# Performance work log

Measured on AMD Instinct MI355X. Metric: run time of the kernel, lower is better.

The kernel has to match this reference:

```python
import jax, jax.numpy as jnp
import numpy as np

TAU = 0.5  # temperature
W_SCALE = 1.0 / np.sqrt(2048.0)  # keep logits in a sane range (like nn.Linear init)


def setup_inputs() -> dict:
    key = jax.random.key(0)
    k1, k2, k3 = jax.random.split(key, 3)
    B, I, O, N = 8192, 2048, 256, 64
    x = jax.random.normal(k1, (B, I), dtype=jnp.float32)
    W = jax.random.normal(k2, (O, N, I), dtype=jnp.float32) * W_SCALE
    b = jnp.zeros((O, N), dtype=jnp.float32)
    grid = jnp.linspace(-1.0, 1.0, N, dtype=jnp.float32)
    # pre-sampled standard Gumbel noise (reparameterized sampling, fixed for determinism)
    u = jax.random.uniform(k3, (B, O, N), dtype=jnp.float32, minval=1e-6, maxval=1.0 - 1e-6)
    gumbel_noise = -jnp.log(-jnp.log(u))
    return {"x": x, "W": W, "b": b, "grid": grid, "gumbel_noise": gumbel_noise}


def reference(x, W, b, grid, gumbel_noise):
    B = x.shape[0]
    O, N, _ = W.shape
    # per-output-feature linears fused into one GEMM; stack(dim=-1) order -> [B, N, O]
    factors = jnp.einsum('bi,oni->bno', x, W) + b.T  # [B, n_bins, out_features]
    # torch .view(B, out_features, n_bins) on the contiguous stacked tensor == reshape
    factors_logits = factors.reshape(B, O, N)
    # gumbel-softmax sampling (soft), then collapse bins onto the value grid
    y = jax.nn.softmax((factors_logits + gumbel_noise) / TAU, axis=-1)  # [B, O, N]
    encoded = jnp.einsum('bon,n->bo', y, grid)  # [B, out_features]
    return (encoded, factors_logits)
```

## Files before the change

kernel.cpp:

```cpp
#include <hip/hip_runtime.h>
#include <hip/hip_bf16.h>
#include <stdint.h>

typedef __bf16 bf16x8 __attribute__((ext_vector_type(8)));
typedef float f32x4 __attribute__((ext_vector_type(4)));
typedef unsigned short u16x8 __attribute__((ext_vector_type(8)));

#define B_ROWS 8192
#define K_DIM  2048
#define O_DIM  256
#define N_BINS 64
#define J_DIM  (O_DIM * N_BINS)
#define NT     (K_DIM / 64)

__device__ __forceinline__ unsigned short f2bf(float f) {
    union { float f; unsigned u; } v; v.f = f;
    unsigned r = (v.u + 0x7fffu + ((v.u >> 16) & 1u)) >> 16;
    return (unsigned short)r;
}

__global__ void cvt_x_kernel(const float* __restrict__ x, unsigned short* __restrict__ xb) {
    int i = (blockIdx.x * 256 + threadIdx.x) * 4;
    float4 v = *(const float4*)(x + i);
    ushort4 o;
    o.x = f2bf(v.x); o.y = f2bf(v.y); o.z = f2bf(v.z); o.w = f2bf(v.w);
    *(ushort4*)(xb + i) = o;
}

__global__ void cvt_w_kernel(const float* __restrict__ W, unsigned short* __restrict__ vb) {
    int bid = blockIdx.x;
    int p   = bid >> 1;
    int i0  = (bid & 1) * 1024 + threadIdx.x * 4;
    int src = (p & (O_DIM - 1)) * (N_BINS * K_DIM) + (p >> 8) * K_DIM + i0;
    float4 v = *(const float4*)(W + src);
    ushort4 o;
    o.x = f2bf(v.x); o.y = f2bf(v.y); o.z = f2bf(v.z); o.w = f2bf(v.w);
    *(ushort4*)(vb + (size_t)p * K_DIM + i0) = o;
}

__device__ __forceinline__ u16x8 pack8(float4 a, float4 b) {
    u16x8 r;
    r[0] = f2bf(a.x); r[1] = f2bf(a.y); r[2] = f2bf(a.z); r[3] = f2bf(a.w);
    r[4] = f2bf(b.x); r[5] = f2bf(b.y); r[6] = f2bf(b.z); r[7] = f2bf(b.w);
    return r;
}

#define GLDS(gsrc, ldst) \
    __builtin_amdgcn_global_load_lds((const __attribute__((address_space(1))) void*)(gsrc), \
                                     (__attribute__((address_space(3))) void*)(ldst), 16, 0, 0)
#define SBAR()   __builtin_amdgcn_s_barrier()
#define SCHED0() __builtin_amdgcn_sched_barrier(0)
#define WAIT_VM(N)   do { asm volatile("s_waitcnt vmcnt(" #N ")" ::: "memory"); } while (0)
#define WAIT_LGKM0() do { asm volatile("s_waitcnt lgkmcnt(0)" ::: "memory"); SCHED0(); } while (0)
#define MFMA(a, b, c) (c) = __builtin_amdgcn_mfma_f32_16x16x32_bf16((a), (b), (c), 0, 0, 0)

__global__ __launch_bounds__(512, 2) void gemm8_kernel(
    const unsigned short* __restrict__ xb,
    const unsigned short* __restrict__ vb,
    const float* __restrict__ bias,
    float* __restrict__ logits)
{
    __shared__ unsigned short As[2][2][256][32];
    __shared__ unsigned short Bs[2][2][256][32];

    const int tid  = threadIdx.x;
    const int lane = tid & 63;
    const int wv   = tid >> 6;
    const int wr   = wv >> 2;
    const int wc   = wv & 3;

    const int bid = blockIdx.x;
    const int swz  = (bid & 7) * 256 + (bid >> 3);
    const int bm   = (swz >> 8) * 4 + (swz & 3);
    const int bn   = (swz & 255) >> 2;
    const int row0 = bm * 256;
    const int col0 = bn * 256;

    const int oss = (tid * 16) ^ (tid & 32);
    const int sr  = oss >> 6;
    const int sc  = (oss >> 1) & 31;

    const unsigned short* gA = xb + (size_t)(row0 + sr) * K_DIM + sc;
    const unsigned short* gB = vb + (size_t)(col0 + sr) * K_DIM + sc;

    auto stageA = [&](int kt, int h, int b) {
        const unsigned short* g = gA + kt * 64 + h * 32;
        unsigned short* l = &As[b][h][0][0] + wv * 512;
        GLDS(g, l);
        GLDS(g + (size_t)128 * K_DIM, l + 4096);
    };
    auto stageB = [&](int kt, int h, int b) {
        const unsigned short* g = gB + kt * 64 + h * 32;
        unsigned short* l = &Bs[b][h][0][0] + wv * 512;
        GLDS(g, l);
        GLDS(g + (size_t)128 * K_DIM, l + 4096);
    };

    const int arb  = wr * 128 + (lane & 15);
    const int brb  = wc * 64 + (lane & 15);
    const int slot = ((lane >> 4) * 8) ^ ((lane & 8) << 1);

    f32x4 acc[8][4];
#pragma unroll
    for (int m = 0; m < 8; ++m)
#pragma unroll
        for (int n = 0; n < 4; ++n)
            acc[m][n] = (f32x4){0.f, 0.f, 0.f, 0.f};

    bf16x8 af[8], b0, b1;

    stageA(0, 0, 0); stageB(0, 0, 0); stageA(0, 1, 0); stageB(0, 1, 0);
    WAIT_VM(4); SCHED0(); SBAR(); SCHED0();

    for (int kt = 0; kt < NT - 1; ++kt) {
        const int cur = kt & 1, nxt = cur ^ 1;
#pragma unroll
        for (int m = 0; m < 8; ++m) af[m] = *(const bf16x8*)&As[cur][0][arb + m * 16][slot];
        b0 = *(const bf16x8*)&Bs[cur][0][brb][slot];
        b1 = *(const bf16x8*)&Bs[cur][0][brb + 16][slot];
        stageA(kt + 1, 0, nxt);
        SBAR(); WAIT_LGKM0();
        __builtin_amdgcn_s_setprio(1);
#pragma unroll
        for (int m = 0; m < 8; ++m) { MFMA(af[m], b0, acc[m][0]); MFMA(af[m], b1, acc[m][1]); }
        __builtin_amdgcn_s_setprio(0);
        SBAR();
        b0 = *(const bf16x8*)&Bs[cur][0][brb + 32][slot];
        b1 = *(const bf16x8*)&Bs[cur][0][brb + 48][slot];
        stageB(kt + 1, 0, nxt);
        WAIT_VM(4); SCHED0(); SBAR(); SCHED0();
        WAIT_LGKM0();
        __builtin_amdgcn_s_setprio(1);
#pragma unroll
        for (int m = 0; m < 8; ++m) { MFMA(af[m], b0, acc[m][2]); MFMA(af[m], b1, acc[m][3]); }
        __builtin_amdgcn_s_setprio(0);
        SBAR();
#pragma unroll
        for (int m = 0; m < 8; ++m) af[m] = *(const bf16x8*)&As[cur][1][arb + m * 16][slot];
        b0 = *(const bf16x8*)&Bs[cur][1][brb + 32][slot];
        b1 = *(const bf16x8*)&Bs[cur][1][brb + 48][slot];
        stageA(kt + 1, 1, nxt);
        SBAR(); WAIT_LGKM0();
        __builtin_amdgcn_s_setprio(1);
#pragma unroll
        for (int m = 0; m < 8; ++m) { MFMA(af[m], b0, acc[m][2]); MFMA(af[m], b1, acc[m][3]); }
        __builtin_amdgcn_s_setprio(0);
        SBAR();
        b0 = *(const bf16x8*)&Bs[cur][1][brb][slot];
        b1 = *(const bf16x8*)&Bs[cur][1][brb + 16][slot];
        stageB(kt + 1, 1, nxt);
        WAIT_VM(4); SCHED0(); SBAR(); SCHED0();
        WAIT_LGKM0();
        __builtin_amdgcn_s_setprio(1);
#pragma unroll
        for (int m = 0; m < 8; ++m) { MFMA(af[m], b0, acc[m][0]); MFMA(af[m], b1, acc[m][1]); }
        __builtin_amdgcn_s_setprio(0);
        SBAR();
    }

    {
        const int cur = (NT - 1) & 1;
#pragma unroll
        for (int m = 0; m < 8; ++m) af[m] = *(const bf16x8*)&As[cur][0][arb + m * 16][slot];
        b0 = *(const bf16x8*)&Bs[cur][0][brb][slot];
        b1 = *(const bf16x8*)&Bs[cur][0][brb + 16][slot];
        SBAR(); WAIT_LGKM0();
        __builtin_amdgcn_s_setprio(1);
#pragma unroll
        for (int m = 0; m < 8; ++m) { MFMA(af[m], b0, acc[m][0]); MFMA(af[m], b1, acc[m][1]); }
        __builtin_amdgcn_s_setprio(0);
        SBAR();
        b0 = *(const bf16x8*)&Bs[cur][0][brb + 32][slot];
        b1 = *(const bf16x8*)&Bs[cur][0][brb + 48][slot];
        WAIT_VM(0); SCHED0(); SBAR(); SCHED0();
        WAIT_LGKM0();
        __builtin_amdgcn_s_setprio(1);
#pragma unroll
        for (int m = 0; m < 8; ++m) { MFMA(af[m], b0, acc[m][2]); MFMA(af[m], b1, acc[m][3]); }
        __builtin_amdgcn_s_setprio(0);
        SBAR();
#pragma unroll
        for (int m = 0; m < 8; ++m) af[m] = *(const bf16x8*)&As[cur][1][arb + m * 16][slot];
        b0 = *(const bf16x8*)&Bs[cur][1][brb + 32][slot];
        b1 = *(const bf16x8*)&Bs[cur][1][brb + 48][slot];
        SBAR(); WAIT_LGKM0();
        __builtin_amdgcn_s_setprio(1);
#pragma unroll
        for (int m = 0; m < 8; ++m) { MFMA(af[m], b0, acc[m][2]); MFMA(af[m], b1, acc[m][3]); }
        __builtin_amdgcn_s_setprio(0);
        SBAR();
        b0 = *(const bf16x8*)&Bs[cur][1][brb][slot];
        b1 = *(const bf16x8*)&Bs[cur][1][brb + 16][slot];
        WAIT_LGKM0();
        __builtin_amdgcn_s_setprio(1);
#pragma unroll
        for (int m = 0; m < 8; ++m) { MFMA(af[m], b0, acc[m][0]); MFMA(af[m], b1, acc[m][1]); }
        __builtin_amdgcn_s_setprio(0);
    }

    const int r_base = row0 + wr * 128 + (lane >> 4) * 4;
    const int c_base = col0 + wc * 64 + (lane & 15);
#pragma unroll
    for (int n = 0; n < 4; ++n) {
        const int c = c_base + n * 16;
        const float bv = bias[(c & (O_DIM - 1)) * N_BINS + (c >> 8)];
#pragma unroll
        for (int m = 0; m < 8; ++m) {
            const int r = r_base + m * 16;
            float* out = logits + (size_t)r * J_DIM + c;
#pragma unroll
            for (int q = 0; q < 4; ++q)
                out[(size_t)q * J_DIM] = acc[m][n][q] + bv;
        }
    }
}

__global__ __launch_bounds__(256) void gemm_fb(
    const float* __restrict__ xf,
    const float* __restrict__ Wf,
    const float* __restrict__ bias,
    float* __restrict__ logits)
{
    __shared__ unsigned short Asm_[128 * 32];
    __shared__ unsigned short Bsm_[128 * 32];

    const int tid = threadIdx.x;
    const int bid = blockIdx.x;
    const int swz = (bid & 7) * 1024 + (bid >> 3);
    const int row0 = (swz >> 7) * 128;
    const int col0 = (swz & 127) * 128;

    const int lane = tid & 63;
    const int wid  = tid >> 6;
    const int wr   = wid >> 1;
    const int wc   = wid & 1;

    f32x4 acc[4][4];
#pragma unroll
    for (int m = 0; m < 4; ++m)
#pragma unroll
        for (int n = 0; n < 4; ++n)
            acc[m][n] = (f32x4){0.f, 0.f, 0.f, 0.f};

    const int srow = tid >> 2;
    const int koff = (tid & 3) * 8;
    const int ra0 = row0 + srow, ra1 = row0 + 64 + srow;
    const int rb0 = col0 + srow, rb1 = col0 + 64 + srow;

    unsigned short* la0 = &Asm_[tid * 8];
    unsigned short* la1 = &Asm_[(256 + tid) * 8];
    unsigned short* lb0 = &Bsm_[tid * 8];
    unsigned short* lb1 = &Bsm_[(256 + tid) * 8];

    const float* fa0 = xf + (size_t)ra0 * K_DIM + koff;
    const float* fa1 = xf + (size_t)ra1 * K_DIM + koff;
    const float* fb0 = Wf + (size_t)((rb0 & (O_DIM - 1)) * (N_BINS * K_DIM) + (rb0 >> 8) * K_DIM) + koff;
    const float* fb1 = Wf + (size_t)((rb1 & (O_DIM - 1)) * (N_BINS * K_DIM) + (rb1 >> 8) * K_DIM) + koff;

    const int a_row  = wr * 64 + (lane & 15);
    const int b_row  = wc * 64 + (lane & 15);
    const int k_half = (lane >> 4) * 8;

    for (int kt = 0; kt < K_DIM / 32; ++kt) {
        const int kbase = kt * 32;
        *(u16x8*)la0 = pack8(*(const float4*)(fa0 + kbase), *(const float4*)(fa0 + kbase + 4));
        *(u16x8*)la1 = pack8(*(const float4*)(fa1 + kbase), *(const float4*)(fa1 + kbase + 4));
        *(u16x8*)lb0 = pack8(*(const float4*)(fb0 + kbase), *(const float4*)(fb0 + kbase + 4));
        *(u16x8*)lb1 = pack8(*(const float4*)(fb1 + kbase), *(const float4*)(fb1 + kbase + 4));
        __syncthreads();
        bf16x8 af[4], bg[4];
#pragma unroll
        for (int m = 0; m < 4; ++m) af[m] = *(const bf16x8*)&Asm_[(a_row + m * 16) * 32 + k_half];
#pragma unroll
        for (int n = 0; n < 4; ++n) bg[n] = *(const bf16x8*)&Bsm_[(b_row + n * 16) * 32 + k_half];
#pragma unroll
        for (int m = 0; m < 4; ++m)
#pragma unroll
            for (int n = 0; n < 4; ++n)
                MFMA(af[m], bg[n], acc[m][n]);
        __syncthreads();
    }

    const int r_base = row0 + wr * 64 + (lane >> 4) * 4;
    const int c_base = col0 + wc * 64 + (lane & 15);
#pragma unroll
    for (int n = 0; n < 4; ++n) {
        const int c = c_base + n * 16;
        const float bv = bias[(c & (O_DIM - 1)) * N_BINS + (c >> 8)];
#pragma unroll
        for (int m = 0; m < 4; ++m) {
            const int r = r_base + m * 16;
            float* out = logits + (size_t)r * J_DIM + c;
#pragma unroll
            for (int q = 0; q < 4; ++q)
                out[(size_t)q * J_DIM] = acc[m][n][q] + bv;
        }
    }
}

__global__ void softmax_encode_kernel(
    const float* __restrict__ logits,
    const float* __restrict__ gumbel,
    const float* __restrict__ grid,
    float* __restrict__ encoded)
{
    int t = blockIdx.x * 256 + threadIdx.x;
    int g = t >> 4;
    int l = t & 15;
    size_t base = (size_t)g * 64 + l * 4;
    float4 L = *(const float4*)(logits + base);
    float4 G = *(const float4*)(gumbel + base);
    float4 gr = *(const float4*)(grid + l * 4);

    float z0 = (L.x + G.x) * 2.0f;
    float z1 = (L.y + G.y) * 2.0f;
    float z2 = (L.z + G.z) * 2.0f;
    float z3 = (L.w + G.w) * 2.0f;

    float m = fmaxf(fmaxf(z0, z1), fmaxf(z2, z3));
#pragma unroll
    for (int s = 1; s < 16; s <<= 1) m = fmaxf(m, __shfl_xor(m, s, 16));

    float e0 = __expf(z0 - m), e1 = __expf(z1 - m), e2 = __expf(z2 - m), e3 = __expf(z3 - m);
    float ssum = e0 + e1 + e2 + e3;
    float dsum = e0 * gr.x + e1 * gr.y + e2 * gr.z + e3 * gr.w;
#pragma unroll
    for (int s = 1; s < 16; s <<= 1) {
        ssum += __shfl_xor(ssum, s, 16);
        dsum += __shfl_xor(dsum, s, 16);
    }
    if (l == 0) encoded[g] = dsum / ssum;
}

extern "C" void kernel_launch(void* const* d_in, const int* in_sizes, int n_in,
                              void* d_out, int out_size, void* d_ws, size_t ws_size,
                              hipStream_t stream) {
    const float* x      = (const float*)d_in[0];
    const float* W      = (const float*)d_in[1];
    const float* bias   = (const float*)d_in[2];
    const float* grid   = (const float*)d_in[3];
    const float* gumbel = (const float*)d_in[4];

    float* encoded = (float*)d_out;
    float* logits  = (float*)d_out + (size_t)B_ROWS * O_DIM;

    const size_t xb_bytes = (size_t)B_ROWS * K_DIM * 2;
    const size_t vb_bytes = (size_t)J_DIM * K_DIM * 2;

    if (ws_size >= xb_bytes + vb_bytes) {
        unsigned short* xb = (unsigned short*)d_ws;
        unsigned short* vb = (unsigned short*)((char*)d_ws + xb_bytes);
        cvt_x_kernel<<<(B_ROWS * K_DIM) / 1024, 256, 0, stream>>>(x, xb);
        cvt_w_kernel<<<J_DIM * 2, 256, 0, stream>>>(W, vb);
        gemm8_kernel<<<(B_ROWS / 256) * (J_DIM / 256), 512, 0, stream>>>(xb, vb, bias, logits);
    } else {
        gemm_fb<<<(B_ROWS / 128) * (J_DIM / 128), 256, 0, stream>>>(x, W, bias, logits);
    }

    softmax_encode_kernel<<<(B_ROWS * O_DIM * 16) / 256, 256, 0, stream>>>(logits, gumbel, grid, encoded);
}
```

Before: 865.3 us.

## Restructure GEMM main loop into 4-stage K32 ring buffer pipeline

Replaces the double-buffered K=64 tile loop (two halves, many barriers) with a 4-slot ring of K=32 tiles, prefetching three tiles ahead and using one barrier per tile. Each K32 step loads A and B fragments, issues the next global-to-LDS stage, and splits the MFMAs into two halves gated by partial lgkmcnt waits. The goal is to cut barrier count and keep more loads in flight to hide memory latency. The LDS footprint stays the same, but the tighter vmcnt accounting and single barrier before overwriting ring slots bring a risk of races or subtle scheduling regressions.

```diff
diff --git a/kernel.cpp b/kernel.cpp
--- a/kernel.cpp
+++ b/kernel.cpp
@@ -11,7 +11,7 @@
 #define O_DIM  256
 #define N_BINS 64
 #define J_DIM  (O_DIM * N_BINS)
-#define NT     (K_DIM / 64)
+#define NT32   (K_DIM / 32)
 
 __device__ __forceinline__ unsigned short f2bf(float f) {
     union { float f; unsigned u; } v; v.f = f;
@@ -51,8 +51,34 @@
 #define SBAR()   __builtin_amdgcn_s_barrier()
 #define SCHED0() __builtin_amdgcn_sched_barrier(0)
 #define WAIT_VM(N)   do { asm volatile("s_waitcnt vmcnt(" #N ")" ::: "memory"); } while (0)
-#define WAIT_LGKM0() do { asm volatile("s_waitcnt lgkmcnt(0)" ::: "memory"); SCHED0(); } while (0)
+#define WAIT_LGKM(N) do { asm volatile("s_waitcnt lgkmcnt(" #N ")" ::: "memory"); SCHED0(); } while (0)
 #define MFMA(a, b, c) (c) = __builtin_amdgcn_mfma_f32_16x16x32_bf16((a), (b), (c), 0, 0, 0)
+
+#define KTILE_BODY(BUF, STAGE_A, STAGE_B) do {                                          \
+    bf16x8 a0_[4], a1_[4], bf_[4];                                                      \
+    _Pragma("unroll") for (int m_ = 0; m_ < 4; ++m_)                                    \
+        a0_[m_] = *(const bf16x8*)&As[BUF][arb + m_ * 16][slot];                        \
+    _Pragma("unroll") for (int n_ = 0; n_ < 4; ++n_)                                    \
+        bf_[n_] = *(const bf16x8*)&Bs[BUF][brb + n_ * 16][slot];                        \
+    _Pragma("unroll") for (int m_ = 0; m_ < 4; ++m_)                                    \
+        a1_[m_] = *(const bf16x8*)&As[BUF][arb + 64 + m_ * 16][slot];                   \
+    STAGE_A;                                                                            \
+    WAIT_LGKM(4);                                                                       \
+    __builtin_amdgcn_s_setprio(1);                                                      \
+    _Pragma("unroll") for (int m_ = 0; m_ < 4; ++m_) {                                  \
+        MFMA(a0_[m_], bf_[0], acc[m_][0]); MFMA(a0_[m_], bf_[1], acc[m_][1]);           \
+        MFMA(a0_[m_], bf_[2], acc[m_][2]); MFMA(a0_[m_], bf_[3], acc[m_][3]);           \
+    }                                                                                   \
+    __builtin_amdgcn_s_setprio(0);                                                      \
+    STAGE_B;                                                                            \
+    WAIT_LGKM(0);                                                                       \
+    __builtin_amdgcn_s_setprio(1);                                                      \
+    _Pragma("unroll") for (int m_ = 0; m_ < 4; ++m_) {                                  \
+        MFMA(a1_[m_], bf_[0], acc[4 + m_][0]); MFMA(a1_[m_], bf_[1], acc[4 + m_][1]);   \
+        MFMA(a1_[m_], bf_[2], acc[4 + m_][2]); MFMA(a1_[m_], bf_[3], acc[4 + m_][3]);   \
+    }                                                                                   \
+    __builtin_amdgcn_s_setprio(0);                                                      \
+} while (0)
 
 __global__ __launch_bounds__(512, 2) void gemm8_kernel(
     const unsigned short* __restrict__ xb,
@@ -60,8 +86,8 @@
     const float* __restrict__ bias,
     float* __restrict__ logits)
 {
-    __shared__ unsigned short As[2][2][256][32];
-    __shared__ unsigned short Bs[2][2][256][32];
+    __shared__ unsigned short As[4][256][32];
+    __shared__ unsigned short Bs[4][256][32];
 
     const int tid  = threadIdx.x;
     const int lane = tid & 63;
@@ -83,15 +109,15 @@
     const unsigned short* gA = xb + (size_t)(row0 + sr) * K_DIM + sc;
     const unsigned short* gB = vb + (size_t)(col0 + sr) * K_DIM + sc;
 
-    auto stageA = [&](int kt, int h, int b) {
-        const unsigned short* g = gA + kt * 64 + h * 32;
-        unsigned short* l = &As[b][h][0][0] + wv * 512;
+    auto stageA = [&](int k, int b) {
+        const unsigned short* g = gA + k * 32;
+        unsigned short* l = &As[b][0][0] + wv * 512;
         GLDS(g, l);
         GLDS(g + (size_t)128 * K_DIM, l + 4096);
     };
-    auto stageB = [&](int kt, int h, int b) {
-        const unsigned short* g = gB + kt * 64 + h * 32;
-        unsigned short* l = &Bs[b][h][0][0] + wv * 512;
+    auto stageB = [&](int k, int b) {
+        const unsigned short* g = gB + k * 32;
+        unsigned short* l = &Bs[b][0][0] + wv * 512;
         GLDS(g, l);
         GLDS(g + (size_t)128 * K_DIM, l + 4096);
     };
@@ -107,96 +133,22 @@
         for (int n = 0; n < 4; ++n)
             acc[m][n] = (f32x4){0.f, 0.f, 0.f, 0.f};
 
-    bf16x8 af[8], b0, b1;
-
-    stageA(0, 0, 0); stageB(0, 0, 0); stageA(0, 1, 0); stageB(0, 1, 0);
-    WAIT_VM(4); SCHED0(); SBAR(); SCHED0();
-
-    for (int kt = 0; kt < NT - 1; ++kt) {
-        const int cur = kt & 1, nxt = cur ^ 1;
-#pragma unroll
-        for (int m = 0; m < 8; ++m) af[m] = *(const bf16x8*)&As[cur][0][arb + m * 16][slot];
-        b0 = *(const bf16x8*)&Bs[cur][0][brb][slot];
-        b1 = *(const bf16x8*)&Bs[cur][0][brb + 16][slot];
-        stageA(kt + 1, 0, nxt);
-        SBAR(); WAIT_LGKM0();
-        __builtin_amdgcn_s_setprio(1);
-#pragma unroll
-        for (int m = 0; m < 8; ++m) { MFMA(af[m], b0, acc[m][0]); MFMA(af[m], b1, acc[m][1]); }
-        __builtin_amdgcn_s_setprio(0);
-        SBAR();
-        b0 = *(const bf16x8*)&Bs[cur][0][brb + 32][slot];
-        b1 = *(const bf16x8*)&Bs[cur][0][brb + 48][slot];
-        stageB(kt + 1, 0, nxt);
-        WAIT_VM(4); SCHED0(); SBAR(); SCHED0();
-        WAIT_LGKM0();
-        __builtin_amdgcn_s_setprio(1);
-#pragma unroll
-        for (int m = 0; m < 8; ++m) { MFMA(af[m], b0, acc[m][2]); MFMA(af[m], b1, acc[m][3]); }
-        __builtin_amdgcn_s_setprio(0);
-        SBAR();
-#pragma unroll
-        for (int m = 0; m < 8; ++m) af[m] = *(const bf16x8*)&As[cur][1][arb + m * 16][slot];
-        b0 = *(const bf16x8*)&Bs[cur][1][brb + 32][slot];
-        b1 = *(const bf16x8*)&Bs[cur][1][brb + 48][slot];
-        stageA(kt + 1, 1, nxt);
-        SBAR(); WAIT_LGKM0();
-        __builtin_amdgcn_s_setprio(1);
-#pragma unroll
-        for (int m = 0; m < 8; ++m) { MFMA(af[m], b0, acc[m][2]); MFMA(af[m], b1, acc[m][3]); }
-        __builtin_amdgcn_s_setprio(0);
-        SBAR();
-        b0 = *(const bf16x8*)&Bs[cur][1][brb][slot];
-        b1 = *(const bf16x8*)&Bs[cur][1][brb + 16][slot];
-        stageB(kt + 1, 1, nxt);
-        WAIT_VM(4); SCHED0(); SBAR(); SCHED0();
-        WAIT_LGKM0();
-        __builtin_amdgcn_s_setprio(1);
-#pragma unroll
-        for (int m = 0; m < 8; ++m) { MFMA(af[m], b0, acc[m][0]); MFMA(af[m], b1, acc[m][1]); }
-        __builtin_amdgcn_s_setprio(0);
-        SBAR();
-    }
-
-    {
-        const int cur = (NT - 1) & 1;
-#pragma unroll
-        for (int m = 0; m < 8; ++m) af[m] = *(const bf16x8*)&As[cur][0][arb + m * 16][slot];
-        b0 = *(const bf16x8*)&Bs[cur][0][brb][slot];
-        b1 = *(const bf16x8*)&Bs[cur][0][brb + 16][slot];
-        SBAR(); WAIT_LGKM0();
-        __builtin_amdgcn_s_setprio(1);
-#pragma unroll
-        for (int m = 0; m < 8; ++m) { MFMA(af[m], b0, acc[m][0]); MFMA(af[m], b1, acc[m][1]); }
-        __builtin_amdgcn_s_setprio(0);
-        SBAR();
-        b0 = *(const bf16x8*)&Bs[cur][0][brb + 32][slot];
-        b1 = *(const bf16x8*)&Bs[cur][0][brb + 48][slot];
-        WAIT_VM(0); SCHED0(); SBAR(); SCHED0();
-        WAIT_LGKM0();
-        __builtin_amdgcn_s_setprio(1);
-#pragma unroll
-        for (int m = 0; m < 8; ++m) { MFMA(af[m], b0, acc[m][2]); MFMA(af[m], b1, acc[m][3]); }
-        __builtin_amdgcn_s_setprio(0);
-        SBAR();
-#pragma unroll
-        for (int m = 0; m < 8; ++m) af[m] = *(const bf16x8*)&As[cur][1][arb + m * 16][slot];
-        b0 = *(const bf16x8*)&Bs[cur][1][brb + 32][slot];
-        b1 = *(const bf16x8*)&Bs[cur][1][brb + 48][slot];
-        SBAR(); WAIT_LGKM0();
-        __builtin_amdgcn_s_setprio(1);
-#pragma unroll
-        for (int m = 0; m < 8; ++m) { MFMA(af[m], b0, acc[m][2]); MFMA(af[m], b1, acc[m][3]); }
-        __builtin_amdgcn_s_setprio(0);
-        SBAR();
-        b0 = *(const bf16x8*)&Bs[cur][1][brb][slot];
-        b1 = *(const bf16x8*)&Bs[cur][1][brb + 16][slot];
-        WAIT_LGKM0();
-        __builtin_amdgcn_s_setprio(1);
-#pragma unroll
-        for (int m = 0; m < 8; ++m) { MFMA(af[m], b0, acc[m][0]); MFMA(af[m], b1, acc[m][1]); }
-        __builtin_amdgcn_s_setprio(0);
-    }
+    stageA(0, 0); stageB(0, 0);
+    stageA(1, 1); stageB(1, 1);
+    stageA(2, 2); stageB(2, 2);
+
+    for (int it = 0; it < 15; ++it) {
+        const int kt0 = it * 4;
+#pragma unroll
+        for (int u = 0; u < 4; ++u) {
+            WAIT_VM(8); SBAR();
+            KTILE_BODY(u, stageA(kt0 + u + 3, (u + 3) & 3), stageB(kt0 + u + 3, (u + 3) & 3));
+        }
+    }
+    WAIT_VM(8); SBAR(); KTILE_BODY(0, stageA(63, 3), stageB(63, 3));
+    WAIT_VM(8); SBAR(); KTILE_BODY(1, (void)0, (void)0);
+    WAIT_VM(4); SBAR(); KTILE_BODY(2, (void)0, (void)0);
+    WAIT_VM(0); SBAR(); KTILE_BODY(3, (void)0, (void)0);
 
     const int r_base = row0 + wr * 128 + (lane >> 4) * 4;
     const int c_base = col0 + wc * 64 + (lane & 15);
```

New measurement: 836.6 us. 1.03x faster.
